# Performance work log

Hardware: AMD Instinct MI355X
Metric: run time of the kernel (lower is better)

The kernel has to match this reference:

```python
import jax, jax.numpy as jnp
import numpy as np

INPUT_DIM = 256
HIDDEN_DIM = 64
BATCH = 1024
N_ITEMS = 200


def setup_inputs() -> dict:
    key = jax.random.key(0)
    k1, k2, k3, k4, k5 = jax.random.split(key, 5)
    item_embedding = jax.random.normal(k1, (BATCH, N_ITEMS, INPUT_DIM), dtype=jnp.float32)
    query_embedding = jax.random.normal(k2, (BATCH, INPUT_DIM), dtype=jnp.float32)
    # query_projection: Linear(input_dim -> input_dim*hidden_dim); xavier-ish scale
    W_q = jax.random.normal(k3, (INPUT_DIM, INPUT_DIM * HIDDEN_DIM), dtype=jnp.float32) * 0.02
    b_q = jax.random.uniform(k4, (INPUT_DIM * HIDDEN_DIM,), dtype=jnp.float32, minval=0.0, maxval=0.01)
    # reduce_projection: Linear(hidden_dim -> 1, bias=False)
    W_r = jax.random.normal(k5, (HIDDEN_DIM,), dtype=jnp.float32) * 0.1
    return {
        "item_embedding": item_embedding,
        "query_embedding": query_embedding,
        "W_q": W_q,
        "b_q": b_q,
        "W_r": W_r,
    }


def reference(item_embedding, query_embedding, W_q, b_q, W_r):
    B = query_embedding.shape[0]
    # linear + tanh, reshape to (B, input_dim, hidden_dim)
    projected_query = jnp.tanh(query_embedding @ W_q + b_q)
    projected_query = projected_query.reshape(B, INPUT_DIM, HIDDEN_DIM)
    # batched einsum: (B, R, I) x (B, I, H) -> (B, R, H)
    dotted = jnp.einsum('bri,bih->brh', item_embedding, projected_query)
    # reduce_projection (H -> 1, no bias): score (B, R)
    score = jnp.einsum('brh,h->br', dotted, W_r)
    # ZAM normalization: exp / (1 + sum exp) over items
    es = jnp.exp(score)
    weight = es / (1.0 + jnp.sum(es, axis=1, keepdims=True))  # (B, R)
    # weighted sum over items -> (B, input_dim)
    entity_embedding = jnp.einsum('br,bri->bi', weight, item_embedding)
    return entity_embedding
```

## Files before the change

### kernel.cpp

```cpp
#include <hip/hip_runtime.h>

#define IDIM   256
#define HDIM   64
#define BATCH  1024
#define NITEMS 200
#define NCOLS  (IDIM * HDIM)

typedef __bf16 bf16x8 __attribute__((ext_vector_type(8)));
typedef float  f32x4  __attribute__((ext_vector_type(4)));

__device__ __forceinline__ unsigned short f2bf(float f) {
    unsigned int u = __float_as_uint(f);
    u += 0x7FFFu + ((u >> 16) & 1u);
    return (unsigned short)(u >> 16);
}

__device__ __forceinline__ float fast_tanh(float x) {
    float e2 = __expf(2.0f * x);
    return 1.0f - 2.0f * __builtin_amdgcn_rcpf(e2 + 1.0f);
}

#define GLOAD_LDS16(g, l) __builtin_amdgcn_global_load_lds(                 \
    (const __attribute__((address_space(1))) void*)(g),                     \
    (__attribute__((address_space(3))) void*)(l), 16, 0, 0)

__global__ __launch_bounds__(256) void k_prep(const float* __restrict__ q,
                                              const float* __restrict__ Wq,
                                              unsigned short* __restrict__ Aq,
                                              unsigned short* __restrict__ Bt) {
    __shared__ float tile[32][33];
    int blk = blockIdx.x;
    int tid = threadIdx.x;
    if (blk >= 4096) {
        int idx = (blk - 4096) * 256 + tid;
        float4 f = ((const float4*)q)[idx];
        ushort4 o;
        o.x = f2bf(f.x); o.y = f2bf(f.y); o.z = f2bf(f.z); o.w = f2bf(f.w);
        ((ushort4*)Aq)[idx] = o;
        return;
    }
    int n0 = (blk & 511) * 32;
    int k0 = (blk >> 9) * 32;
    int tx = tid & 31;
    int ty = tid >> 5;
#pragma unroll
    for (int j = 0; j < 32; j += 8)
        tile[ty + j][tx] = Wq[(size_t)(k0 + ty + j) * NCOLS + n0 + tx];
    __syncthreads();
#pragma unroll
    for (int j = 0; j < 32; j += 8)
        Bt[(size_t)(n0 + ty + j) * IDIM + k0 + tx] = f2bf(tile[tx][ty + j]);
}

__global__ __launch_bounds__(256) void k_gemm_v(const unsigned short* __restrict__ Aq,
                                                const unsigned short* __restrict__ Bt,
                                                const float* __restrict__ bq,
                                                const float* __restrict__ Wr,
                                                float* __restrict__ V) {
    __shared__ __align__(16) unsigned short As[128 * 32];
    __shared__ __align__(16) unsigned short Bs[128 * 32];
    int tid  = threadIdx.x;
    int w    = tid >> 6;
    int lane = tid & 63;
    int l16  = lane & 15;
    int quad = lane >> 4;
    int blk  = blockIdx.x;
    int bn   = blk & 127;
    int bm   = blk >> 7;

    int m_off  = (w & 1) * 64;
    int n_off  = (w >> 1) * 64;
    int n_base = bn * 128 + n_off;
    int icol   = bn * 2 + (w >> 1);

    const unsigned short* Ag = Aq + (size_t)(bm * 128 + (tid >> 2)) * IDIM + (tid & 3) * 8;
    const unsigned short* Bg = Bt + (size_t)(bn * 128 + (tid >> 2)) * IDIM + (tid & 3) * 8;
    unsigned short* Asl = As + tid * 8;
    unsigned short* Bsl = Bs + tid * 8;

    const unsigned short* Asp = As + (m_off + l16) * 32 + quad * 8;
    const unsigned short* Bsp = Bs + (n_off + l16) * 32 + quad * 8;

    float bv[4], wr[4];
#pragma unroll
    for (int nt = 0; nt < 4; nt++) {
        int nl = nt * 16 + l16;
        bv[nt] = bq[n_base + nl];
        wr[nt] = Wr[nl];
    }

    f32x4 acc[4][4] = {};
#pragma unroll
    for (int kk = 0; kk < IDIM; kk += 32) {
        GLOAD_LDS16(Ag + kk,             Asl);
        GLOAD_LDS16(Ag + 64 * IDIM + kk, Asl + 2048);
        GLOAD_LDS16(Bg + kk,             Bsl);
        GLOAD_LDS16(Bg + 64 * IDIM + kk, Bsl + 2048);
        __syncthreads();
        bf16x8 a[4], b[4];
#pragma unroll
        for (int t = 0; t < 4; t++) a[t] = *(const bf16x8*)(Asp + t * 16 * 32);
#pragma unroll
        for (int t = 0; t < 4; t++) b[t] = *(const bf16x8*)(Bsp + t * 16 * 32);
#pragma unroll
        for (int mt = 0; mt < 4; mt++)
#pragma unroll
            for (int nt = 0; nt < 4; nt++)
                acc[mt][nt] = __builtin_amdgcn_mfma_f32_16x16x32_bf16(a[mt], b[nt], acc[mt][nt], 0, 0, 0);
        __syncthreads();
    }

#pragma unroll
    for (int mt = 0; mt < 4; mt++) {
#pragma unroll
        for (int reg = 0; reg < 4; reg++) {
            float s = 0.0f;
#pragma unroll
            for (int nt = 0; nt < 4; nt++) {
                float c = acc[mt][nt][reg] + bv[nt];
                s += fast_tanh(c) * wr[nt];
            }
            s += __shfl_xor(s, 1);
            s += __shfl_xor(s, 2);
            s += __shfl_xor(s, 4);
            s += __shfl_xor(s, 8);
            if (l16 == 0) {
                int m = bm * 128 + m_off + mt * 16 + quad * 4 + reg;
                V[m * IDIM + icol] = s;
            }
        }
    }
}

__global__ __launch_bounds__(256) void k_score(const float* __restrict__ item,
                                               const float* __restrict__ V,
                                               float* __restrict__ out) {
    __shared__ float lacc[16][IDIM];
    __shared__ float lS[16];
    int b    = blockIdx.x;
    int tid  = threadIdx.x;
    int wid  = tid >> 6;
    int lane = tid & 63;
    int l16  = lane & 15;
    int quad = lane >> 4;

    const float4* itemB = (const float4*)(item + (size_t)b * NITEMS * IDIM);
    const float4* Vb    = (const float4*)(V + (size_t)b * IDIM);

    float4 v[4];
#pragma unroll
    for (int c = 0; c < 4; c++) v[c] = Vb[l16 + 16 * c];

    float4 acc[4];
#pragma unroll
    for (int c = 0; c < 4; c++) acc[c] = make_float4(0.f, 0.f, 0.f, 0.f);
    float S = 0.f;

    for (int chunk = wid; chunk < 25; chunk += 4) {
        int r0 = chunk * 8 + quad;
        int r1 = r0 + 4;
        float4 x0[4], x1[4];
#pragma unroll
        for (int c = 0; c < 4; c++) x0[c] = itemB[(size_t)r0 * 64 + l16 + 16 * c];
#pragma unroll
        for (int c = 0; c < 4; c++) x1[c] = itemB[(size_t)r1 * 64 + l16 + 16 * c];

        float d0 = 0.f, d1 = 0.f;
#pragma unroll
        for (int c = 0; c < 4; c++) {
            d0 += x0[c].x * v[c].x + x0[c].y * v[c].y + x0[c].z * v[c].z + x0[c].w * v[c].w;
            d1 += x1[c].x * v[c].x + x1[c].y * v[c].y + x1[c].z * v[c].z + x1[c].w * v[c].w;
        }
#pragma unroll
        for (int m = 1; m < 16; m <<= 1) {
            d0 += __shfl_xor(d0, m);
            d1 += __shfl_xor(d1, m);
        }
        float e0 = __expf(d0);
        float e1 = __expf(d1);
        S += e0 + e1;
#pragma unroll
        for (int c = 0; c < 4; c++) {
            acc[c].x += e0 * x0[c].x + e1 * x1[c].x;
            acc[c].y += e0 * x0[c].y + e1 * x1[c].y;
            acc[c].z += e0 * x0[c].z + e1 * x1[c].z;
            acc[c].w += e0 * x0[c].w + e1 * x1[c].w;
        }
    }

    int row = wid * 4 + quad;
#pragma unroll
    for (int c = 0; c < 4; c++)
        ((float4*)&lacc[row][0])[l16 + 16 * c] = acc[c];
    if (l16 == 0) lS[row] = S;
    __syncthreads();

    float s = 0.f;
#pragma unroll
    for (int i = 0; i < 16; i++) s += lacc[i][tid];
    float Stot = 0.f;
#pragma unroll
    for (int i = 0; i < 16; i++) Stot += lS[i];
    out[(size_t)b * IDIM + tid] = s / (1.0f + Stot);
}

extern "C" void kernel_launch(void* const* d_in, const int* in_sizes, int n_in,
                              void* d_out, int out_size, void* d_ws, size_t ws_size,
                              hipStream_t stream) {
    const float* item  = (const float*)d_in[0];
    const float* query = (const float*)d_in[1];
    const float* Wq    = (const float*)d_in[2];
    const float* bq    = (const float*)d_in[3];
    const float* Wr    = (const float*)d_in[4];
    float* out = (float*)d_out;

    char* ws = (char*)d_ws;
    unsigned short* Aq = (unsigned short*)ws;
    unsigned short* Bt = (unsigned short*)(ws + (512 << 10));
    float*          V  = (float*)(ws + (512 << 10) + (8 << 20));

    k_prep  <<<4352, 256, 0, stream>>>(query, Wq, Aq, Bt);
    k_gemm_v<<<1024, 256, 0, stream>>>(Aq, Bt, bq, Wr, V);
    k_score <<<1024, 256, 0, stream>>>(item, V, out);
}
```

Measured before the change: 328.5 us.

## Double-buffer GEMM LDS tiles, vectorize Wq transpose, use DPP row reductions

The projection GEMM now uses two LDS buffers, so the next K-slice is loaded asynchronously while MFMAs run on the current one. This removes one barrier per iteration and hides load latency. The Wq transpose in the prep kernel reads float4 and writes packed bf16 pairs to cut memory transactions. Both the GEMM epilogue and the score kernel replace 16-lane shuffle-xor reductions with DPP row_ror adds, which avoids LDS-based shuffles. The cost is doubled LDS use in the GEMM kernel, which could reduce occupancy.

```diff
diff --git a/kernel.cpp b/kernel.cpp
--- a/kernel.cpp
+++ b/kernel.cpp
@@ -19,6 +19,17 @@
     float e2 = __expf(2.0f * x);
     return 1.0f - 2.0f * __builtin_amdgcn_rcpf(e2 + 1.0f);
 }
+
+template <int CTRL>
+__device__ __forceinline__ float row_ror_add(float x) {
+    return x + __int_as_float(__builtin_amdgcn_update_dpp(
+        0, __float_as_int(x), CTRL, 0xF, 0xF, false));
+}
+#define ROW_REDUCE16(d)                 \
+    d = row_ror_add<0x121>(d);          \
+    d = row_ror_add<0x122>(d);          \
+    d = row_ror_add<0x124>(d);          \
+    d = row_ror_add<0x128>(d);
 
 #define GLOAD_LDS16(g, l) __builtin_amdgcn_global_load_lds(                 \
     (const __attribute__((address_space(1))) void*)(g),                     \
@@ -41,15 +52,21 @@
     }
     int n0 = (blk & 511) * 32;
     int k0 = (blk >> 9) * 32;
-    int tx = tid & 31;
-    int ty = tid >> 5;
-#pragma unroll
-    for (int j = 0; j < 32; j += 8)
-        tile[ty + j][tx] = Wq[(size_t)(k0 + ty + j) * NCOLS + n0 + tx];
+    int ty4 = tid >> 3;
+    int tx4 = (tid & 7) * 4;
+    float4 f = *(const float4*)&Wq[(size_t)(k0 + ty4) * NCOLS + n0 + tx4];
+    tile[ty4][tx4 + 0] = f.x; tile[ty4][tx4 + 1] = f.y;
+    tile[ty4][tx4 + 2] = f.z; tile[ty4][tx4 + 3] = f.w;
     __syncthreads();
-#pragma unroll
-    for (int j = 0; j < 32; j += 8)
-        Bt[(size_t)(n0 + ty + j) * IDIM + k0 + tx] = f2bf(tile[tx][ty + j]);
+    int txk = (tid & 15) * 2;
+    int tyr = tid >> 4;
+#pragma unroll
+    for (int j = 0; j < 32; j += 16) {
+        ushort2 o;
+        o.x = f2bf(tile[txk][tyr + j]);
+        o.y = f2bf(tile[txk + 1][tyr + j]);
+        *(ushort2*)&Bt[(size_t)(n0 + tyr + j) * IDIM + k0 + txk] = o;
+    }
 }
 
 __global__ __launch_bounds__(256) void k_gemm_v(const unsigned short* __restrict__ Aq,
@@ -57,8 +74,8 @@
                                                 const float* __restrict__ bq,
                                                 const float* __restrict__ Wr,
                                                 float* __restrict__ V) {
-    __shared__ __align__(16) unsigned short As[128 * 32];
-    __shared__ __align__(16) unsigned short Bs[128 * 32];
+    __shared__ __align__(16) unsigned short As[2][128 * 32];
+    __shared__ __align__(16) unsigned short Bs[2][128 * 32];
     int tid  = threadIdx.x;
     int w    = tid >> 6;
     int lane = tid & 63;
@@ -75,11 +92,13 @@
 
     const unsigned short* Ag = Aq + (size_t)(bm * 128 + (tid >> 2)) * IDIM + (tid & 3) * 8;
     const unsigned short* Bg = Bt + (size_t)(bn * 128 + (tid >> 2)) * IDIM + (tid & 3) * 8;
-    unsigned short* Asl = As + tid * 8;
-    unsigned short* Bsl = Bs + tid * 8;
-
-    const unsigned short* Asp = As + (m_off + l16) * 32 + quad * 8;
-    const unsigned short* Bsp = Bs + (n_off + l16) * 32 + quad * 8;
+
+#define STAGE(buf, kk) do {                                                \
+        GLOAD_LDS16(Ag + (kk) * 32,             &As[buf][tid * 8]);        \
+        GLOAD_LDS16(Ag + 64 * IDIM + (kk) * 32, &As[buf][2048 + tid * 8]); \
+        GLOAD_LDS16(Bg + (kk) * 32,             &Bs[buf][tid * 8]);        \
+        GLOAD_LDS16(Bg + 64 * IDIM + (kk) * 32, &Bs[buf][2048 + tid * 8]); \
+    } while (0)
 
     float bv[4], wr[4];
 #pragma unroll
@@ -90,13 +109,14 @@
     }
 
     f32x4 acc[4][4] = {};
-#pragma unroll
-    for (int kk = 0; kk < IDIM; kk += 32) {
-        GLOAD_LDS16(Ag + kk,             Asl);
-        GLOAD_LDS16(Ag + 64 * IDIM + kk, Asl + 2048);
-        GLOAD_LDS16(Bg + kk,             Bsl);
-        GLOAD_LDS16(Bg + 64 * IDIM + kk, Bsl + 2048);
-        __syncthreads();
+    STAGE(0, 0);
+    __syncthreads();
+#pragma unroll
+    for (int kk = 0; kk < 8; kk++) {
+        int cur = kk & 1;
+        if (kk < 7) STAGE(cur ^ 1, kk + 1);
+        const unsigned short* Asp = &As[cur][(m_off + l16) * 32 + quad * 8];
+        const unsigned short* Bsp = &Bs[cur][(n_off + l16) * 32 + quad * 8];
         bf16x8 a[4], b[4];
 #pragma unroll
         for (int t = 0; t < 4; t++) a[t] = *(const bf16x8*)(Asp + t * 16 * 32);
@@ -109,7 +129,9 @@
                 acc[mt][nt] = __builtin_amdgcn_mfma_f32_16x16x32_bf16(a[mt], b[nt], acc[mt][nt], 0, 0, 0);
         __syncthreads();
     }
-
+#undef STAGE
+
+    int i = icol;
 #pragma unroll
     for (int mt = 0; mt < 4; mt++) {
 #pragma unroll
@@ -120,13 +142,10 @@
                 float c = acc[mt][nt][reg] + bv[nt];
                 s += fast_tanh(c) * wr[nt];
             }
-            s += __shfl_xor(s, 1);
-            s += __shfl_xor(s, 2);
-            s += __shfl_xor(s, 4);
-            s += __shfl_xor(s, 8);
+            ROW_REDUCE16(s);
             if (l16 == 0) {
                 int m = bm * 128 + m_off + mt * 16 + quad * 4 + reg;
-                V[m * IDIM + icol] = s;
+                V[m * IDIM + i] = s;
             }
         }
     }
@@ -171,11 +190,8 @@
             d0 += x0[c].x * v[c].x + x0[c].y * v[c].y + x0[c].z * v[c].z + x0[c].w * v[c].w;
             d1 += x1[c].x * v[c].x + x1[c].y * v[c].y + x1[c].z * v[c].z + x1[c].w * v[c].w;
         }
-#pragma unroll
-        for (int m = 1; m < 16; m <<= 1) {
-            d0 += __shfl_xor(d0, m);
-            d1 += __shfl_xor(d1, m);
-        }
+        ROW_REDUCE16(d0);
+        ROW_REDUCE16(d1);
         float e0 = __expf(d0);
         float e1 = __expf(d1);
         S += e0 + e1;
```

Result: no change. 324.3 us (-1.3%).
